# Kernel tuning notes

Measured on AMD Instinct MI355X. Metric: run time of the kernel, lower is better.

## Reference

```python
import jax, jax.numpy as jnp
import numpy as np

B, T, D, H, V, L = 2, 1024, 512, 8, 50257, 4
HD = D // H  # head size
FF = 4 * D


def _ln(x, w, b):
    mu = jnp.mean(x, axis=-1, keepdims=True)
    var = jnp.mean((x - mu) ** 2, axis=-1, keepdims=True)
    return (x - mu) * jax.lax.rsqrt(var + 1e-5) * w + b


def setup_inputs() -> dict:
    key = jax.random.key(0)
    ks = jax.random.split(key, 12)
    s = 0.02
    return {
        "idx": jax.random.randint(ks[0], (B, T), 0, V),
        "tok_emb": jax.random.normal(ks[1], (V, D)) * s,
        "pos_emb": jax.random.normal(ks[2], (T, D)) * s,
        "Wq": jax.random.normal(ks[3], (L, H, D, HD)) * s,
        "Wk": jax.random.normal(ks[4], (L, H, D, HD)) * s,
        "Wv": jax.random.normal(ks[5], (L, H, D, HD)) * s,
        "Wo": jax.random.normal(ks[6], (L, D, D)) * s,
        "bo": jnp.zeros((L, D)),
        "W1": jax.random.normal(ks[7], (L, D, FF)) * s,
        "b1": jnp.zeros((L, FF)),
        "W2": jax.random.normal(ks[8], (L, FF, D)) * s,
        "b2": jnp.zeros((L, D)),
        "ln1_w": jnp.ones((L, D)), "ln1_b": jnp.zeros((L, D)),
        "ln2_w": jnp.ones((L, D)), "ln2_b": jnp.zeros((L, D)),
        "Wlm": jax.random.normal(ks[9], (D, V)) * s,
        "blm": jnp.zeros((V,)),
    }


def reference(idx, tok_emb, pos_emb, Wq, Wk, Wv, Wo, bo, W1, b1, W2, b2,
              ln1_w, ln1_b, ln2_w, ln2_b, Wlm, blm):
    b, t = idx.shape
    x = tok_emb[idx] + pos_emb[:t]  # [B,T,D]
    mask = jnp.tril(jnp.ones((t, t), dtype=bool))
    scale = D ** (-0.5)  # NOTE: original scales by full n_embd, not head_size
    for l in range(L):
        # pre-norm that also feeds the residual (x = ln1(x); x = x + sa(x))
        h = _ln(x, ln1_w[l], ln1_b[l])
        q = jnp.einsum('btd,hdk->bhtk', h, Wq[l])
        k = jnp.einsum('btd,hdk->bhtk', h, Wk[l])
        v = jnp.einsum('btd,hdk->bhtk', h, Wv[l])
        wei = jnp.einsum('bhtk,bhsk->bhts', q, k) * scale
        wei = jnp.where(mask, wei, -jnp.inf)
        wei = jax.nn.softmax(wei, axis=-1)  # dropout omitted (eval mode)
        att = jnp.einsum('bhts,bhsk->bhtk', wei, v)
        att = att.transpose(0, 2, 1, 3).reshape(b, t, D)  # concat heads
        x = h + att @ Wo[l] + bo[l]
        h2 = _ln(x, ln2_w[l], ln2_b[l])
        x = h2 + jax.nn.relu(h2 @ W1[l] + b1[l]) @ W2[l] + b2[l]
    logits = x @ Wlm + blm  # [B,T,V]
    return logits
```

## Files before the change

### kernel.cpp

```cpp
#include <hip/hip_runtime.h>
#include <hip/hip_bf16.h>

typedef __hip_bfloat16 bf16;
typedef __attribute__((ext_vector_type(8))) short s8v;
typedef __attribute__((ext_vector_type(4))) float f4v;

#define B_ 2
#define T_ 1024
#define D_ 512
#define H_ 8
#define HD_ 64
#define V_ 50257
#define VPAD_ 50304
#define L_ 4
#define FF_ 2048
#define BT_ (B_*T_)

__device__ __forceinline__ float ldw(const void* p, size_t i, int f32m) {
  return f32m ? ((const float*)p)[i] : __bfloat162float(((const bf16*)p)[i]);
}

__device__ __forceinline__ void gload_lds16(const void* g, void* l) {
  __builtin_amdgcn_global_load_lds((const __attribute__((address_space(1))) void*)g,
                                   (__attribute__((address_space(3))) void*)l, 16, 0, 0);
}

__global__ void detect_kernel(const void* __restrict__ ln1w, int* __restrict__ flag) {
  unsigned u = *(const unsigned*)ln1w;
  *flag = (u == 0x3F800000u) ? 1 : 0;
}

__global__ void embed_kernel(const int* __restrict__ idx, const void* __restrict__ tok,
                             const void* __restrict__ pos, float* __restrict__ x,
                             const int* __restrict__ flag) {
  int f32m = *flag;
  int i = blockIdx.x * 256 + threadIdx.x;
  int bt = i >> 9;
  int d  = i & (D_ - 1);
  int t  = bt & (T_ - 1);
  int tk = idx[bt];
  x[i] = ldw(tok, (size_t)tk * D_ + d, f32m) + ldw(pos, (size_t)t * D_ + d, f32m);
}

__global__ void ln_kernel(const float* __restrict__ x, const void* __restrict__ w,
                          const void* __restrict__ b, size_t eoff,
                          bf16* __restrict__ hb, float* __restrict__ hf,
                          const int* __restrict__ flag) {
  int f32m = *flag;
  int t = blockIdx.x;
  int tid = threadIdx.x;
  const float* row = x + (size_t)t * D_;
  float v0 = row[tid], v1 = row[tid + 256];
  __shared__ float red[256];
  red[tid] = v0 + v1;
  __syncthreads();
  for (int s = 128; s > 0; s >>= 1) { if (tid < s) red[tid] += red[tid + s]; __syncthreads(); }
  float mu = red[0] * (1.f / D_);
  __syncthreads();
  float d0 = v0 - mu, d1 = v1 - mu;
  red[tid] = d0 * d0 + d1 * d1;
  __syncthreads();
  for (int s = 128; s > 0; s >>= 1) { if (tid < s) red[tid] += red[tid + s]; __syncthreads(); }
  float rs = rsqrtf(red[0] * (1.f / D_) + 1e-5f);
  float o0 = d0 * rs * ldw(w, eoff + tid, f32m)       + ldw(b, eoff + tid, f32m);
  float o1 = d1 * rs * ldw(w, eoff + tid + 256, f32m) + ldw(b, eoff + tid + 256, f32m);
  size_t base = (size_t)t * D_;
  hf[base + tid] = o0;        hf[base + tid + 256] = o1;
  hb[base + tid] = __float2bfloat16(o0);
  hb[base + tid + 256] = __float2bfloat16(o1);
}

__global__ void repack_qkv_kernel(const void* __restrict__ Wq, const void* __restrict__ Wk,
                                  const void* __restrict__ Wv, size_t eoff,
                                  bf16* __restrict__ out, const int* __restrict__ flag) {
  int f32m = *flag;
  int i = blockIdx.x * 256 + threadIdx.x;
  int n = i >> 9, k = i & 511;
  int sel = n >> 9; int cc = n & 511; int hh = cc >> 6; int hd = cc & 63;
  const void* src = (sel == 0) ? Wq : (sel == 1) ? Wk : Wv;
  out[i] = __float2bfloat16(ldw(src, eoff + ((size_t)hh * D_ + k) * HD_ + hd, f32m));
}

__global__ void transpose_kernel(const void* __restrict__ in, size_t eoff,
                                 bf16* __restrict__ out, int K, int Nin,
                                 const int* __restrict__ flag) {
  int f32m = *flag;
  __shared__ bf16 tl[32][33];
  int n0 = blockIdx.x * 32, k0 = blockIdx.y * 32;
  int tx = threadIdx.x & 31, ty = threadIdx.x >> 5;
#pragma unroll
  for (int i = 0; i < 4; ++i) {
    int k = k0 + ty + i * 8;
    int n = n0 + tx;
    float v = (n < Nin) ? ldw(in, eoff + (size_t)k * Nin + n, f32m) : 0.f;
    tl[ty + i * 8][tx] = __float2bfloat16(v);
  }
  __syncthreads();
#pragma unroll
  for (int i = 0; i < 4; ++i) {
    int n = n0 + ty + i * 8;
    out[(size_t)n * K + k0 + tx] = tl[tx][ty + i * 8];
  }
}

template<int OUTM, int BIAS, int RES, int RELU>
__global__ __launch_bounds__(256)
void mfma_gemm(const bf16* __restrict__ A, const bf16* __restrict__ Bt,
               void* __restrict__ Cout, const void* __restrict__ bias, size_t bieoff,
               const float* __restrict__ res, const int* __restrict__ flag,
               int M, int Nc, int K) {
  __shared__ __align__(16) short As[2][4096];
  __shared__ __align__(16) short Bs[2][4096];
  const int tid = threadIdx.x;
  const int brow = blockIdx.y * 128;
  const int bcol = blockIdx.x * 128;
  const int w = tid >> 6, lane = tid & 63;
  const int wr = w >> 1, wc = w & 1;
  const int lr = lane & 15, lk = lane >> 4;

  const int e0 = tid * 8, e1 = 2048 + tid * 8;
  const int r0 = e0 >> 5, r1 = e1 >> 5;
  const int c0 = (e0 & 31) ^ ((r0 & 3) << 3);
  const int c1 = (e1 & 31) ^ ((r1 & 3) << 3);
  const bf16* ag0 = A + (size_t)(brow + r0) * K + c0;
  const bf16* ag1 = A + (size_t)(brow + r1) * K + c1;
  const bf16* bg0 = Bt + (size_t)(bcol + r0) * K + c0;
  const bf16* bg1 = Bt + (size_t)(bcol + r1) * K + c1;

  int aoff[4], boff[4];
#pragma unroll
  for (int i = 0; i < 4; ++i) {
    int ra = wr * 64 + i * 16 + lr;
    aoff[i] = ra * 32 + ((lk * 8) ^ ((lr & 3) << 3));
    int rb = wc * 64 + i * 16 + lr;
    boff[i] = rb * 32 + ((lk * 8) ^ ((lr & 3) << 3));
  }

  f4v acc[4][4];
  const f4v z = {0.f, 0.f, 0.f, 0.f};
#pragma unroll
  for (int i = 0; i < 4; ++i)
#pragma unroll
    for (int j = 0; j < 4; ++j) acc[i][j] = z;

  const int nt = K >> 5;
  gload_lds16(ag0, &As[0][e0]); gload_lds16(ag1, &As[0][e1]);
  gload_lds16(bg0, &Bs[0][e0]); gload_lds16(bg1, &Bs[0][e1]);

  for (int kt = 0; kt < nt; ++kt) {
    __syncthreads();
    const int cur = kt & 1;
    if (kt + 1 < nt) {
      const size_t ko = (size_t)(kt + 1) * 32;
      gload_lds16(ag0 + ko, &As[cur ^ 1][e0]);
      gload_lds16(ag1 + ko, &As[cur ^ 1][e1]);
      gload_lds16(bg0 + ko, &Bs[cur ^ 1][e0]);
      gload_lds16(bg1 + ko, &Bs[cur ^ 1][e1]);
    }
    s8v a[4], b[4];
#pragma unroll
    for (int i = 0; i < 4; ++i) a[i] = *(const s8v*)&As[cur][aoff[i]];
#pragma unroll
    for (int i = 0; i < 4; ++i) b[i] = *(const s8v*)&Bs[cur][boff[i]];
#pragma unroll
    for (int mi = 0; mi < 4; ++mi)
#pragma unroll
      for (int ni = 0; ni < 4; ++ni)
        acc[mi][ni] = __builtin_amdgcn_mfma_f32_16x16x32_bf16(a[mi], b[ni], acc[mi][ni], 0, 0, 0);
  }

  const int f32m = *flag;
#pragma unroll
  for (int mi = 0; mi < 4; ++mi) {
    const int row = brow + wr * 64 + mi * 16 + lk * 4;
#pragma unroll
    for (int ni = 0; ni < 4; ++ni) {
      const int col = bcol + wc * 64 + ni * 16 + lr;
      if (col < Nc) {
        float bv = BIAS ? ldw(bias, bieoff + col, f32m) : 0.f;
#pragma unroll
        for (int rr = 0; rr < 4; ++rr) {
          float v = acc[mi][ni][rr] + bv;
          size_t ci = (size_t)(row + rr) * Nc + col;
          if (RES) v += res[ci];
          if (RELU) v = fmaxf(v, 0.f);
          if (OUTM == 0) ((float*)Cout)[ci] = v;
          else if (OUTM == 1) ((bf16*)Cout)[ci] = __float2bfloat16(v);
          else { if (f32m) ((float*)Cout)[ci] = v;
                 else ((bf16*)Cout)[ci] = __float2bfloat16(v); }
        }
      }
    }
  }
}

#define ATT_SCALE 0.044194173824159216f
__global__ __launch_bounds__(128) void fattn_kernel(const bf16* __restrict__ qkv,
                                                    bf16* __restrict__ att) {
  const int tid = threadIdx.x;
  const int w = tid >> 6, lane = tid & 63;
  const int lr = lane & 15, lk = lane >> 4;
  const int sx = blockIdx.x;
  const int strip = (sx & 1) ? (31 - (sx >> 1)) : (sx >> 1);
  const int s0 = strip * 32;
  const int hh = blockIdx.y, b = blockIdx.z;
  const int q0w = s0 + w * 16;

  __shared__ __align__(16) short Klds[64 * 64];
  __shared__ __align__(16) short Vt[64 * 72];
  __shared__ __align__(16) short Pl[2][16 * 72];
  unsigned* vt32 = (unsigned*)Vt;

  const bf16* qbase = qkv + (size_t)(b * T_ + q0w + lr) * 1536 + hh * 64;
  s8v qf[2];
#pragma unroll
  for (int kk = 0; kk < 2; ++kk)
    qf[kk] = *(const s8v*)(qbase + kk * 32 + lk * 8);

  const bf16* kg = qkv + (size_t)b * T_ * 1536 + 512 + hh * 64;
  const bf16* vg = kg + 512;

  f4v acc_o[4];
  const f4v z4 = {0.f, 0.f, 0.f, 0.f};
#pragma unroll
  for (int dt = 0; dt < 4; ++dt) acc_o[dt] = z4;
  float m[4], l[4];
#pragma unroll
  for (int r = 0; r < 4; ++r) { m[r] = -1e30f; l[r] = 0.f; }

  const int jmax = (s0 + 31) >> 6;
  for (int jt = 0; jt <= jmax; ++jt) {
    __syncthreads();
    const bf16* kt = kg + (size_t)jt * 64 * 1536;
#pragma unroll
    for (int c = 0; c < 4; ++c) {
      int e = tid * 8 + c * 1024;
      int row = e >> 6, col = e & 63;
      int colw = col ^ ((row & 7) << 3);
      gload_lds16(kt + (size_t)row * 1536 + colw, &Klds[e]);
    }
    const bf16* vgt = vg + (size_t)jt * 64 * 1536;
#pragma unroll
    for (int u = 0; u < 2; ++u) {
      int unit = tid * 2 + u;
      int kp = unit >> 3, cc = (unit & 7) * 8;
      s8v v0 = *(const s8v*)(vgt + (size_t)(2 * kp) * 1536 + cc);
      s8v v1 = *(const s8v*)(vgt + (size_t)(2 * kp + 1) * 1536 + cc);
#pragma unroll
      for (int j = 0; j < 8; ++j) {
        unsigned pk = (unsigned)(unsigned short)v0[j] |
                      ((unsigned)(unsigned short)v1[j] << 16);
        vt32[(cc + j) * 36 + kp] = pk;
      }
    }
    __syncthreads();

    if (jt * 64 <= q0w + 15) {
      const bool diag = (jt == jmax);
      f4v s[4];
#pragma unroll
      for (int nt = 0; nt < 4; ++nt) s[nt] = z4;
#pragma unroll
      for (int kk = 0; kk < 2; ++kk)
#pragma unroll
        for (int nt = 0; nt < 4; ++nt) {
          int row = nt * 16 + lr;
          const s8v kf = *(const s8v*)&Klds[row * 64 +
                           ((kk * 32 + lk * 8) ^ ((lr & 7) << 3))];
          s[nt] = __builtin_amdgcn_mfma_f32_16x16x32_bf16(qf[kk], kf, s[nt], 0, 0, 0);
        }
      float pv[4][4];
#pragma unroll
      for (int nt = 0; nt < 4; ++nt)
#pragma unroll
        for (int r = 0; r < 4; ++r) {
          float v = s[nt][r] * ATT_SCALE;
          if (diag && (jt * 64 + nt * 16 + lr > q0w + lk * 4 + r)) v = -1e30f;
          pv[nt][r] = v;
        }
#pragma unroll
      for (int r = 0; r < 4; ++r) {
        float mm = fmaxf(fmaxf(pv[0][r], pv[1][r]), fmaxf(pv[2][r], pv[3][r]));
        mm = fmaxf(mm, __shfl_xor(mm, 1));
        mm = fmaxf(mm, __shfl_xor(mm, 2));
        mm = fmaxf(mm, __shfl_xor(mm, 4));
        mm = fmaxf(mm, __shfl_xor(mm, 8));
        float nm = fmaxf(m[r], mm);
        float cf = __expf(m[r] - nm);
        m[r] = nm;
        float ls = 0.f;
#pragma unroll
        for (int nt = 0; nt < 4; ++nt) {
          float p = __expf(pv[nt][r] - nm);
          pv[nt][r] = p;
          ls += p;
        }
        ls += __shfl_xor(ls, 1); ls += __shfl_xor(ls, 2);
        ls += __shfl_xor(ls, 4); ls += __shfl_xor(ls, 8);
        l[r] = l[r] * cf + ls;
#pragma unroll
        for (int dt = 0; dt < 4; ++dt) acc_o[dt][r] *= cf;
      }
      bf16* pw = (bf16*)&Pl[w][0];
#pragma unroll
      for (int nt = 0; nt < 4; ++nt)
#pragma unroll
        for (int r = 0; r < 4; ++r)
          pw[(lk * 4 + r) * 72 + nt * 16 + lr] = __float2bfloat16(pv[nt][r]);
#pragma unroll
      for (int kk = 0; kk < 2; ++kk) {
        const s8v pa = *(const s8v*)&Pl[w][lr * 72 + kk * 32 + lk * 8];
#pragma unroll
        for (int dt = 0; dt < 4; ++dt) {
          const s8v vf = *(const s8v*)&Vt[(dt * 16 + lr) * 72 + kk * 32 + lk * 8];
          acc_o[dt] = __builtin_amdgcn_mfma_f32_16x16x32_bf16(pa, vf, acc_o[dt], 0, 0, 0);
        }
      }
    }
  }

#pragma unroll
  for (int dt = 0; dt < 4; ++dt)
#pragma unroll
    for (int r = 0; r < 4; ++r) {
      int q = q0w + lk * 4 + r;
      float v = acc_o[dt][r] / l[r];
      att[(size_t)(b * T_ + q) * D_ + hh * 64 + dt * 16 + lr] = __float2bfloat16(v);
    }
}

__global__ void cast_kernel(const float* __restrict__ x, bf16* __restrict__ xb) {
  int i = blockIdx.x * 256 + threadIdx.x;
  xb[i] = __float2bfloat16(x[i]);
}

__global__ void lm_fallback_kernel(const float* __restrict__ A, const void* __restrict__ Bw,
                                   void* __restrict__ Cout, const void* __restrict__ bias,
                                   const int* __restrict__ flag, int M, int N, int K) {
  const int f32m = *flag;
  __shared__ __align__(16) float As[16][72];
  __shared__ __align__(16) float Bs[16][72];
  const int tid = threadIdx.x;
  const int brow = blockIdx.y * 64;
  const int bcol = blockIdx.x * 64;
  const int tr = tid >> 4, tc = tid & 15;
  float acc[4][4] = {};
  for (int k0 = 0; k0 < K; k0 += 16) {
#pragma unroll
    for (int i = 0; i < 4; ++i) {
      int e = tid + i * 256;
      int r = e >> 4, c = e & 15;
      As[c][r] = A[(size_t)(brow + r) * K + k0 + c];
    }
#pragma unroll
    for (int i = 0; i < 4; ++i) {
      int e = tid + i * 256;
      int r = e >> 6, c = e & 63;
      int col = bcol + c;
      Bs[r][c] = (col < N) ? ldw(Bw, (size_t)(k0 + r) * N + col, f32m) : 0.f;
    }
    __syncthreads();
#pragma unroll
    for (int kk = 0; kk < 16; ++kk) {
      const float4 av = *reinterpret_cast<const float4*>(&As[kk][tr * 4]);
      const float4 bv = *reinterpret_cast<const float4*>(&Bs[kk][tc * 4]);
      float a_[4] = {av.x, av.y, av.z, av.w};
      float b_[4] = {bv.x, bv.y, bv.z, bv.w};
#pragma unroll
      for (int i = 0; i < 4; ++i)
#pragma unroll
        for (int j = 0; j < 4; ++j) acc[i][j] += a_[i] * b_[j];
    }
    __syncthreads();
  }
#pragma unroll
  for (int i = 0; i < 4; ++i) {
    int row = brow + tr * 4 + i;
#pragma unroll
    for (int j = 0; j < 4; ++j) {
      int col = bcol + tc * 4 + j;
      if (col < N) {
        float v = acc[i][j] + ldw(bias, col, f32m);
        if (f32m) ((float*)Cout)[(size_t)row * N + col] = v;
        else      ((bf16*) Cout)[(size_t)row * N + col] = __float2bfloat16(v);
      }
    }
  }
}

template<int OUTM, int BI, int RE, int RL>
static void launch_mfma(const bf16* A, const bf16* Bt, void* C, const void* bias,
                        size_t bieoff, const float* res, const int* flag,
                        int M, int Nc, int Npad, int K, hipStream_t s) {
  dim3 grid(Npad / 128, M / 128);
  mfma_gemm<OUTM, BI, RE, RL><<<grid, 256, 0, s>>>(A, Bt, C, bias, bieoff, res, flag, M, Nc, K);
}

extern "C" void kernel_launch(void* const* d_in, const int* in_sizes, int n_in,
                              void* d_out, int out_size, void* d_ws, size_t ws_size,
                              hipStream_t stream) {
  const int*  idx  = (const int*) d_in[0];
  const void* tok  = d_in[1];
  const void* pos  = d_in[2];
  const void* Wq   = d_in[3];
  const void* Wk   = d_in[4];
  const void* Wv   = d_in[5];
  const void* Wo   = d_in[6];
  const void* bo   = d_in[7];
  const void* W1   = d_in[8];
  const void* b1   = d_in[9];
  const void* W2   = d_in[10];
  const void* b2   = d_in[11];
  const void* ln1w = d_in[12];
  const void* ln1b = d_in[13];
  const void* ln2w = d_in[14];
  const void* ln2b = d_in[15];
  const void* Wlm  = d_in[16];
  const void* blm  = d_in[17];

  char* p = (char*)d_ws;
  int*   flag = (int*)p;            p += 256;
  float* x    = (float*)p;          p += (size_t)BT_ * D_ * 4;
  float* hf   = (float*)p;          p += (size_t)BT_ * D_ * 4;
  bf16*  h    = (bf16*)p;           p += (size_t)BT_ * D_ * 2;
  bf16*  R    = (bf16*)p;           p += (size_t)BT_ * FF_ * 2;
  bf16*  wrep = (bf16*)p;           p += (size_t)FF_ * D_ * 2;
  bf16*  wlm  = (bf16*)p;           size_t base = (size_t)(p - (char*)d_ws);
  size_t need = base + (size_t)VPAD_ * D_ * 2;
  const bool big = ws_size >= need;

  bf16* qkv = R;
  bf16* att = R + (size_t)BT_ * 1536;
  bf16* ff  = R;
  bf16* xb  = h;

  detect_kernel<<<1, 1, 0, stream>>>(ln1w, flag);
  embed_kernel<<<BT_ * D_ / 256, 256, 0, stream>>>(idx, tok, pos, x, flag);

  for (int l = 0; l < L_; ++l) {
    ln_kernel<<<BT_, 256, 0, stream>>>(x, ln1w, ln1b, (size_t)l * D_, h, hf, flag);
    repack_qkv_kernel<<<1536 * 512 / 256, 256, 0, stream>>>(
        Wq, Wk, Wv, (size_t)l * H_ * D_ * HD_, wrep, flag);
    launch_mfma<1,0,0,0>(h, wrep, qkv, nullptr, 0, nullptr, flag, BT_, 1536, 1536, 512, stream);
    fattn_kernel<<<dim3(32, H_, B_), 128, 0, stream>>>(qkv, att);
    transpose_kernel<<<dim3(16, 16), 256, 0, stream>>>(Wo, (size_t)l * D_ * D_, wrep, 512, 512, flag);
    launch_mfma<0,1,1,0>(att, wrep, x, bo, (size_t)l * D_, hf, flag, BT_, 512, 512, 512, stream);
    ln_kernel<<<BT_, 256, 0, stream>>>(x, ln2w, ln2b, (size_t)l * D_, h, hf, flag);
    transpose_kernel<<<dim3(64, 16), 256, 0, stream>>>(W1, (size_t)l * D_ * FF_, wrep, 512, 2048, flag);
    launch_mfma<1,1,0,1>(h, wrep, ff, b1, (size_t)l * FF_, nullptr, flag, BT_, 2048, 2048, 512, stream);
    transpose_kernel<<<dim3(16, 64), 256, 0, stream>>>(W2, (size_t)l * FF_ * D_, wrep, 2048, 512, flag);
    launch_mfma<0,1,1,0>(ff, wrep, x, b2, (size_t)l * D_, hf, flag, BT_, 512, 512, 2048, stream);
  }

  if (big) {
    cast_kernel<<<BT_ * D_ / 256, 256, 0, stream>>>(x, xb);
    transpose_kernel<<<dim3(VPAD_ / 32, 16), 256, 0, stream>>>(Wlm, 0, wlm, 512, V_, flag);
    launch_mfma<2,1,0,0>(xb, wlm, d_out, blm, 0, nullptr, flag, BT_, V_, VPAD_, 512, stream);
  } else {
    lm_fallback_kernel<<<dim3((V_ + 63) / 64, BT_ / 64), 256, 0, stream>>>(
        x, Wlm, d_out, blm, flag, BT_, V_, 512);
  }
}
```

Baseline: 922.2 us.

## Use 64x64 MFMA tiles for layer GEMMs and swizzled block order for LM head

Adds a 64x64-tile MFMA GEMM for the per-layer projections, which launches more blocks for the small M=2048 GEMMs and so fills more compute units. Adds a dedicated LM-head GEMM that takes a 1D grid and remaps block IDs so that blocks running together share A row tiles and nearby weight columns, aiming at better L2 reuse. VPAD grows to 51200 so the column tiles divide evenly into the remap (8×50 groups). The cost is more padded weight transpose work, plus smaller tiles with lower arithmetic intensity per block.

```diff
diff --git a/kernel.cpp b/kernel.cpp
--- a/kernel.cpp
+++ b/kernel.cpp
@@ -11,7 +11,7 @@
 #define H_ 8
 #define HD_ 64
 #define V_ 50257
-#define VPAD_ 50304
+#define VPAD_ 51200
 #define L_ 4
 #define FF_ 2048
 #define BT_ (B_*T_)
@@ -105,15 +105,99 @@
 
 template<int OUTM, int BIAS, int RES, int RELU>
 __global__ __launch_bounds__(256)
-void mfma_gemm(const bf16* __restrict__ A, const bf16* __restrict__ Bt,
-               void* __restrict__ Cout, const void* __restrict__ bias, size_t bieoff,
-               const float* __restrict__ res, const int* __restrict__ flag,
-               int M, int Nc, int K) {
+void mfma_gemm64(const bf16* __restrict__ A, const bf16* __restrict__ Bt,
+                 void* __restrict__ Cout, const void* __restrict__ bias, size_t bieoff,
+                 const float* __restrict__ res, const int* __restrict__ flag,
+                 int M, int Nc, int K) {
+  __shared__ __align__(16) short As[2][2048];
+  __shared__ __align__(16) short Bs[2][2048];
+  const int tid = threadIdx.x;
+  const int brow = blockIdx.x * 64;
+  const int bcol = blockIdx.y * 64;
+  const int w = tid >> 6, lane = tid & 63;
+  const int wr = w >> 1, wc = w & 1;
+  const int lr = lane & 15, lk = lane >> 4;
+
+  const int e0 = tid * 8;
+  const int r0 = e0 >> 5;
+  const int c0 = (e0 & 31) ^ ((r0 & 3) << 3);
+  const bf16* ag0 = A + (size_t)(brow + r0) * K + c0;
+  const bf16* bg0 = Bt + (size_t)(bcol + r0) * K + c0;
+
+  int aoff[2], boff[2];
+#pragma unroll
+  for (int i = 0; i < 2; ++i) {
+    int ra = wr * 32 + i * 16 + lr;
+    aoff[i] = ra * 32 + ((lk * 8) ^ ((lr & 3) << 3));
+    int rb = wc * 32 + i * 16 + lr;
+    boff[i] = rb * 32 + ((lk * 8) ^ ((lr & 3) << 3));
+  }
+
+  f4v acc[2][2];
+  const f4v z = {0.f, 0.f, 0.f, 0.f};
+#pragma unroll
+  for (int i = 0; i < 2; ++i)
+#pragma unroll
+    for (int j = 0; j < 2; ++j) acc[i][j] = z;
+
+  const int nt = K >> 5;
+  gload_lds16(ag0, &As[0][e0]);
+  gload_lds16(bg0, &Bs[0][e0]);
+
+  for (int kt = 0; kt < nt; ++kt) {
+    __syncthreads();
+    const int cur = kt & 1;
+    if (kt + 1 < nt) {
+      const size_t ko = (size_t)(kt + 1) * 32;
+      gload_lds16(ag0 + ko, &As[cur ^ 1][e0]);
+      gload_lds16(bg0 + ko, &Bs[cur ^ 1][e0]);
+    }
+    s8v a[2], b[2];
+#pragma unroll
+    for (int i = 0; i < 2; ++i) a[i] = *(const s8v*)&As[cur][aoff[i]];
+#pragma unroll
+    for (int i = 0; i < 2; ++i) b[i] = *(const s8v*)&Bs[cur][boff[i]];
+#pragma unroll
+    for (int mi = 0; mi < 2; ++mi)
+#pragma unroll
+      for (int ni = 0; ni < 2; ++ni)
+        acc[mi][ni] = __builtin_amdgcn_mfma_f32_16x16x32_bf16(a[mi], b[ni], acc[mi][ni], 0, 0, 0);
+  }
+
+  const int f32m = *flag;
+#pragma unroll
+  for (int mi = 0; mi < 2; ++mi) {
+    const int row = brow + wr * 32 + mi * 16 + lk * 4;
+#pragma unroll
+    for (int ni = 0; ni < 2; ++ni) {
+      const int col = bcol + wc * 32 + ni * 16 + lr;
+      if (col < Nc) {
+        float bv = BIAS ? ldw(bias, bieoff + col, f32m) : 0.f;
+#pragma unroll
+        for (int rr = 0; rr < 4; ++rr) {
+          float v = acc[mi][ni][rr] + bv;
+          size_t ci = (size_t)(row + rr) * Nc + col;
+          if (RES) v += res[ci];
+          if (RELU) v = fmaxf(v, 0.f);
+          if (OUTM == 0) ((float*)Cout)[ci] = v;
+          else           ((bf16*)Cout)[ci] = __float2bfloat16(v);
+        }
+      }
+    }
+  }
+}
+
+__global__ __launch_bounds__(256)
+void mfma_gemm_lm(const bf16* __restrict__ A, const bf16* __restrict__ Bt,
+                  void* __restrict__ Cout, const void* __restrict__ bias,
+                  const int* __restrict__ flag, int M, int Nc, int K) {
   __shared__ __align__(16) short As[2][4096];
   __shared__ __align__(16) short Bs[2][4096];
+  const int bid = blockIdx.x;
+  const int g = bid >> 3;
+  const int brow = (g & 15) * 128;
+  const int bcol = ((bid & 7) * 50 + (g >> 4)) * 128;
   const int tid = threadIdx.x;
-  const int brow = blockIdx.y * 128;
-  const int bcol = blockIdx.x * 128;
   const int w = tid >> 6, lane = tid & 63;
   const int wr = w >> 1, wc = w & 1;
   const int lr = lane & 15, lk = lane >> 4;
@@ -177,17 +261,13 @@
     for (int ni = 0; ni < 4; ++ni) {
       const int col = bcol + wc * 64 + ni * 16 + lr;
       if (col < Nc) {
-        float bv = BIAS ? ldw(bias, bieoff + col, f32m) : 0.f;
+        float bv = ldw(bias, col, f32m);
 #pragma unroll
         for (int rr = 0; rr < 4; ++rr) {
           float v = acc[mi][ni][rr] + bv;
           size_t ci = (size_t)(row + rr) * Nc + col;
-          if (RES) v += res[ci];
-          if (RELU) v = fmaxf(v, 0.f);
-          if (OUTM == 0) ((float*)Cout)[ci] = v;
-          else if (OUTM == 1) ((bf16*)Cout)[ci] = __float2bfloat16(v);
-          else { if (f32m) ((float*)Cout)[ci] = v;
-                 else ((bf16*)Cout)[ci] = __float2bfloat16(v); }
+          if (f32m) ((float*)Cout)[ci] = v;
+          else      ((bf16*)Cout)[ci] = __float2bfloat16(v);
         }
       }
     }
@@ -389,11 +469,11 @@
 }
 
 template<int OUTM, int BI, int RE, int RL>
-static void launch_mfma(const bf16* A, const bf16* Bt, void* C, const void* bias,
-                        size_t bieoff, const float* res, const int* flag,
-                        int M, int Nc, int Npad, int K, hipStream_t s) {
-  dim3 grid(Npad / 128, M / 128);
-  mfma_gemm<OUTM, BI, RE, RL><<<grid, 256, 0, s>>>(A, Bt, C, bias, bieoff, res, flag, M, Nc, K);
+static void launch_g64(const bf16* A, const bf16* Bt, void* C, const void* bias,
+                       size_t bieoff, const float* res, const int* flag,
+                       int M, int Nc, int Npad, int K, hipStream_t s) {
+  dim3 grid(M / 64, Npad / 64);
+  mfma_gemm64<OUTM, BI, RE, RL><<<grid, 256, 0, s>>>(A, Bt, C, bias, bieoff, res, flag, M, Nc, K);
 }
 
 extern "C" void kernel_launch(void* const* d_in, const int* in_sizes, int n_in,
@@ -441,21 +521,22 @@
     ln_kernel<<<BT_, 256, 0, stream>>>(x, ln1w, ln1b, (size_t)l * D_, h, hf, flag);
     repack_qkv_kernel<<<1536 * 512 / 256, 256, 0, stream>>>(
         Wq, Wk, Wv, (size_t)l * H_ * D_ * HD_, wrep, flag);
-    launch_mfma<1,0,0,0>(h, wrep, qkv, nullptr, 0, nullptr, flag, BT_, 1536, 1536, 512, stream);
+    launch_g64<1,0,0,0>(h, wrep, qkv, nullptr, 0, nullptr, flag, BT_, 1536, 1536, 512, stream);
     fattn_kernel<<<dim3(32, H_, B_), 128, 0, stream>>>(qkv, att);
     transpose_kernel<<<dim3(16, 16), 256, 0, stream>>>(Wo, (size_t)l * D_ * D_, wrep, 512, 512, flag);
-    launch_mfma<0,1,1,0>(att, wrep, x, bo, (size_t)l * D_, hf, flag, BT_, 512, 512, 512, stream);
+    launch_g64<0,1,1,0>(att, wrep, x, bo, (size_t)l * D_, hf, flag, BT_, 512, 512, 512, stream);
     ln_kernel<<<BT_, 256, 0, stream>>>(x, ln2w, ln2b, (size_t)l * D_, h, hf, flag);
     transpose_kernel<<<dim3(64, 16), 256, 0, stream>>>(W1, (size_t)l * D_ * FF_, wrep, 512, 2048, flag);
-    launch_mfma<1,1,0,1>(h, wrep, ff, b1, (size_t)l * FF_, nullptr, flag, BT_, 2048, 2048, 512, stream);
+    launch_g64<1,1,0,1>(h, wrep, ff, b1, (size_t)l * FF_, nullptr, flag, BT_, 2048, 2048, 512, stream);
     transpose_kernel<<<dim3(16, 64), 256, 0, stream>>>(W2, (size_t)l * FF_ * D_, wrep, 2048, 512, flag);
-    launch_mfma<0,1,1,0>(ff, wrep, x, b2, (size_t)l * D_, hf, flag, BT_, 512, 512, 2048, stream);
+    launch_g64<0,1,1,0>(ff, wrep, x, b2, (size_t)l * D_, hf, flag, BT_, 512, 512, 2048, stream);
   }
 
   if (big) {
     cast_kernel<<<BT_ * D_ / 256, 256, 0, stream>>>(x, xb);
     transpose_kernel<<<dim3(VPAD_ / 32, 16), 256, 0, stream>>>(Wlm, 0, wlm, 512, V_, flag);
-    launch_mfma<2,1,0,0>(xb, wlm, d_out, blm, 0, nullptr, flag, BT_, V_, VPAD_, 512, stream);
+    mfma_gemm_lm<<<(BT_ / 128) * (VPAD_ / 128) , 256, 0, stream>>>(
+        xb, wlm, d_out, blm, flag, BT_, V_, 512);
   } else {
     lm_fallback_kernel<<<dim3((V_ + 63) / 64, BT_ / 64), 256, 0, stream>>>(
         x, Wlm, d_out, blm, flag, BT_, V_, 512);
```

After: 820.0 us. -11.1%, faster.
